# Optimization experiments

Measured on AMD Instinct MI355X. Metric: run time of the kernel, lower is better.

## Reference

```python
import jax, jax.numpy as jnp
import numpy as np
import math

B, S, E, H, L, FF = 32, 512, 256, 8, 4, 1024
DH = E // H
EPS = 1e-5


def layernorm(x):
    # nn.LayerNorm(elementwise_affine=False)
    m = jnp.mean(x, axis=-1, keepdims=True)
    v = jnp.mean((x - m) ** 2, axis=-1, keepdims=True)
    return (x - m) / jnp.sqrt(v + EPS)


def make_pos_embedding(e):
    vals = [math.sin(1 / 10000 ** ((i - 1) / e)) if i % 2 == 1
            else math.cos(i / 10000 ** ((i - 1) / e)) for i in range(e)]
    return jnp.asarray(np.array(vals, dtype=np.float32))


def setup_inputs() -> dict:
    key = jax.random.key(0)
    ks = jax.random.split(key, 8)
    sc = 0.02
    x = jax.random.normal(ks[0], (B, S, E), dtype=jnp.float32)
    Wq = jax.random.normal(ks[1], (L, H, DH, DH), dtype=jnp.float32) * sc
    Wk = jax.random.normal(ks[2], (L, H, DH, DH), dtype=jnp.float32) * sc
    Wv = jax.random.normal(ks[3], (L, H, DH, DH), dtype=jnp.float32) * sc
    W1 = jax.random.normal(ks[4], (L, E, FF), dtype=jnp.float32) * sc
    b1 = jnp.zeros((L, FF), dtype=jnp.float32)
    W2 = jax.random.normal(ks[5], (L, FF, E), dtype=jnp.float32) * sc
    b2 = jnp.zeros((L, E), dtype=jnp.float32)
    pos = make_pos_embedding(E)
    return {"x": x, "pos": pos, "Wq": Wq, "Wk": Wk, "Wv": Wv,
            "W1": W1, "b1": b1, "W2": W2, "b2": b2}


def encoder_layer(x, wq, wk, wv, w1, bb1, w2, bb2):
    xn = layernorm(x)
    xh = xn.reshape(B, S, H, DH)  # split embedding into per-head chunks
    q = jnp.einsum('bshd,hde->bhse', xh, wq)
    k = jnp.einsum('bshd,hde->bhse', xh, wk)
    v = jnp.einsum('bshd,hde->bhse', xh, wv)
    scores = jnp.einsum('bhsd,bhtd->bhst', q, k) / jnp.sqrt(jnp.float32(DH))
    a = jax.nn.softmax(scores, axis=-1)
    o = jnp.einsum('bhst,bhtd->bhsd', a, v)
    mha = o.transpose(0, 2, 1, 3).reshape(B, S, E)  # concat heads
    res = mha + x
    rn = layernorm(res)
    ffn = jax.nn.gelu(rn @ w1 + bb1, approximate=False) @ w2 + bb2
    return ffn + res


def reference(x, pos, Wq, Wk, Wv, W1, b1, W2, b2):
    h = x + pos  # fixed sinusoidal positional embedding
    for l in range(L):
        h = encoder_layer(h, Wq[l], Wk[l], Wv[l], W1[l], b1[l], W2[l], b2[l])
    return h
```

## Files before the change

### kernel.cpp

```cpp
#include <hip/hip_runtime.h>
#include <math.h>

#define BB   32
#define SS   512
#define EE   256
#define HH   8
#define LL   4
#define FFD  1024
#define DHD  32

constexpr float LN_EPS = 1e-5f;
constexpr int   NBSE   = BB * SS * EE;

typedef float  f32x4  __attribute__((ext_vector_type(4)));
typedef __bf16 bf16;
typedef __bf16 bf16x4 __attribute__((ext_vector_type(4)));
typedef __bf16 bf16x8 __attribute__((ext_vector_type(8)));

#define WAITV(n) asm volatile("s_waitcnt vmcnt(" #n ")" ::: "memory")

__device__ __forceinline__ void glds16(const bf16* g, bf16* l) {
    __builtin_amdgcn_global_load_lds(
        (const __attribute__((address_space(1))) void*)g,
        (__attribute__((address_space(3))) void*)l,
        16, 0, 0);
}

__device__ __forceinline__ float gelu_f(float x) {
    float u = x * x;
    float t = 1.5957691216057308f * x * (1.0f + 0.044715f * u);
    return x / (1.0f + __expf(-t));
}

__global__ __launch_bounds__(256) void k_prep(const float* __restrict__ W1,
                                              const float* __restrict__ W2,
                                              const float* __restrict__ Wq,
                                              const float* __restrict__ Wk,
                                              const float* __restrict__ Wv,
                                              bf16* __restrict__ W1t,
                                              bf16* __restrict__ W2t,
                                              bf16* __restrict__ Wqt,
                                              bf16* __restrict__ Wkt,
                                              bf16* __restrict__ Wvt) {
    __shared__ float tile[32][33];
    int bid = blockIdx.x;
    int tx = threadIdx.x & 31, ty = threadIdx.x >> 5;
    if (bid < 2048) {
        bool isw2 = bid >= 1024;
        int id = isw2 ? bid - 1024 : bid;
        int K = isw2 ? FFD : EE, N = isw2 ? EE : FFD;
        int l = id >> 8, rem = id & 255;
        int n0, k0;
        if (isw2) { n0 = (rem & 7) * 32;  k0 = (rem >> 3) * 32; }
        else      { n0 = (rem & 31) * 32; k0 = (rem >> 5) * 32; }
        const float* in = (isw2 ? W2 : W1) + (size_t)l * K * N;
        bf16* out       = (isw2 ? W2t : W1t) + (size_t)l * K * N;
        #pragma unroll
        for (int i = 0; i < 32; i += 8)
            tile[ty + i][tx] = in[(size_t)(k0 + ty + i) * N + n0 + tx];
        __syncthreads();
        #pragma unroll
        for (int i = 0; i < 32; i += 8)
            out[(size_t)(n0 + ty + i) * K + k0 + tx] = (bf16)tile[tx][ty + i];
    } else {
        int id = bid - 2048;
        int lh = id & 31, z = id >> 5;
        const float* in = (z == 0 ? Wq : z == 1 ? Wk : Wv) + (size_t)lh * 1024;
        bf16* out       = (z == 0 ? Wqt : z == 1 ? Wkt : Wvt) + (size_t)lh * 1024;
        float scale = (z == 0) ? 0.17677669529663687f : 1.0f;
        #pragma unroll
        for (int i = 0; i < 32; i += 8)
            tile[ty + i][tx] = in[(ty + i) * 32 + tx];
        __syncthreads();
        #pragma unroll
        for (int i = 0; i < 32; i += 8)
            out[(ty + i) * 32 + tx] = (bf16)(tile[tx][ty + i] * scale);
    }
}

template <bool ADDPOS>
__global__ __launch_bounds__(256) void k_lnqkv(const float* __restrict__ xin,
                                               const float* __restrict__ pos,
                                               float* __restrict__ hout,
                                               const bf16* __restrict__ Wqt,
                                               const bf16* __restrict__ Wkt,
                                               const bf16* __restrict__ Wvt,
                                               bf16* __restrict__ qb,
                                               bf16* __restrict__ kb,
                                               bf16* __restrict__ vb) {
    __shared__ __attribute__((aligned(16))) bf16 Xs[32 * 264];
    int b = blockIdx.x, s0 = blockIdx.y * 32;
    int tid = threadIdx.x, w = tid >> 6, lane = tid & 63;
    size_t rowoff = ((size_t)(b * SS + s0 + w * 8)) * EE + lane * 4;
    const float* hb = xin + rowoff;
    float4 pv;
    if (ADDPOS) pv = *(const float4*)(pos + lane * 4);
    float4 xr[8];
    #pragma unroll
    for (int i = 0; i < 8; i++)
        xr[i] = *(const float4*)(hb + (size_t)i * EE);
    if (ADDPOS) {
        #pragma unroll
        for (int i = 0; i < 8; i++) {
            xr[i].x += pv.x; xr[i].y += pv.y; xr[i].z += pv.z; xr[i].w += pv.w;
            *(float4*)(hout + rowoff + (size_t)i * EE) = xr[i];
        }
    }
    #pragma unroll
    for (int i = 0; i < 8; i++) {
        float4 v4 = xr[i];
        float sum = v4.x + v4.y + v4.z + v4.w;
        #pragma unroll
        for (int m = 1; m <= 32; m <<= 1) sum += __shfl_xor(sum, m, 64);
        float mean = sum * (1.0f / EE);
        float dx = v4.x - mean, dy = v4.y - mean, dz = v4.z - mean, dw = v4.w - mean;
        float ss = dx * dx + dy * dy + dz * dz + dw * dw;
        #pragma unroll
        for (int m = 1; m <= 32; m <<= 1) ss += __shfl_xor(ss, m, 64);
        float rstd = rsqrtf(ss * (1.0f / EE) + LN_EPS);
        bf16x4 o4 = { (bf16)(dx * rstd), (bf16)(dy * rstd), (bf16)(dz * rstd), (bf16)(dw * rstd) };
        *(bf16x4*)&Xs[(w * 8 + i) * 264 + lane * 4] = o4;
    }
    __syncthreads();
    int col = lane & 15, quad = lane >> 4;
    int rt = w & 1, hgrp = w >> 1;
    #pragma unroll
    for (int hh2 = 0; hh2 < 4; hh2++) {
        int h = hgrp * 4 + hh2;
        bf16x8 a = *(const bf16x8*)&Xs[(rt * 16 + col) * 264 + h * 32 + quad * 8];
        size_t base = ((size_t)((b * HH + h) * SS) + s0 + rt * 16) * DHD;
        #pragma unroll
        for (int nt = 0; nt < 2; nt++) {
            int e = nt * 16 + col;
            bf16x8 bq  = *(const bf16x8*)(Wqt + (h * 32 + e) * 32 + quad * 8);
            bf16x8 bk2 = *(const bf16x8*)(Wkt + (h * 32 + e) * 32 + quad * 8);
            bf16x8 bv2 = *(const bf16x8*)(Wvt + (h * 32 + e) * 32 + quad * 8);
            f32x4 z = {0.f, 0.f, 0.f, 0.f};
            f32x4 cq = __builtin_amdgcn_mfma_f32_16x16x32_bf16(bq, a, z, 0, 0, 0);
            f32x4 ck = __builtin_amdgcn_mfma_f32_16x16x32_bf16(bk2, a, z, 0, 0, 0);
            f32x4 cv = __builtin_amdgcn_mfma_f32_16x16x32_bf16(a, bv2, z, 0, 0, 0);
            bf16x4 q4 = { (bf16)cq[0], (bf16)cq[1], (bf16)cq[2], (bf16)cq[3] };
            bf16x4 k4 = { (bf16)ck[0], (bf16)ck[1], (bf16)ck[2], (bf16)ck[3] };
            size_t tb = base + (size_t)col * DHD + nt * 16 + quad * 4;
            *(bf16x4*)&qb[tb] = q4;
            *(bf16x4*)&kb[tb] = k4;
            bf16x4 vv = { (bf16)cv[0], (bf16)cv[1], (bf16)cv[2], (bf16)cv[3] };
            *(bf16x4*)&vb[(((size_t)(b * HH + h)) * DHD + e) * SS + s0 + rt * 16 + quad * 4] = vv;
        }
    }
}

#define ATT_LDK 40
#define ATT_LDV 264
#define ATT_LDP 36
__global__ __launch_bounds__(256) void k_attn(const bf16* __restrict__ Q,
                                              const bf16* __restrict__ K,
                                              const bf16* __restrict__ VT,
                                              bf16* __restrict__ O) {
    __shared__ __attribute__((aligned(16))) bf16 Ks[256 * ATT_LDK];
    __shared__ __attribute__((aligned(16))) bf16 Vs[32 * ATT_LDV];
    __shared__ __attribute__((aligned(16))) bf16 Ps[4][16 * ATT_LDP];
    int bh = blockIdx.x;
    int q0 = blockIdx.y * 128;
    int tid = threadIdx.x;
    int w = tid >> 6, lane = tid & 63;
    int col = lane & 15, quad = lane >> 4;
    bf16x8 aq[2];
    #pragma unroll
    for (int sub = 0; sub < 2; sub++)
        aq[sub] = *(const bf16x8*)(Q + ((size_t)(bh * SS + q0 + sub * 64 + w * 16 + col)) * DHD + quad * 8);
    float lr[2] = {0.f, 0.f};
    f32x4 oacc[2][2] = {};
    int ksr = tid >> 2, ksc = (tid & 3) * 8;
    int vd  = tid >> 5, vso = (tid & 31) * 8;
    bf16x8 kr[4], vr[4];
    #pragma unroll
    for (int it = 0; it < 4; it++) {
        kr[it] = *(const bf16x8*)(K + ((size_t)(bh * SS + it * 64 + ksr)) * DHD + ksc);
        vr[it] = *(const bf16x8*)(VT + (((size_t)bh * DHD + it * 8 + vd) * SS) + vso);
    }
    for (int ph = 0; ph < 2; ph++) {
        __syncthreads();
        #pragma unroll
        for (int it = 0; it < 4; it++) {
            *(bf16x8*)&Ks[(it * 64 + ksr) * ATT_LDK + ksc] = kr[it];
            *(bf16x8*)&Vs[(it * 8 + vd) * ATT_LDV + vso] = vr[it];
        }
        if (ph == 0) {
            #pragma unroll
            for (int it = 0; it < 4; it++) {
                kr[it] = *(const bf16x8*)(K + ((size_t)(bh * SS + 256 + it * 64 + ksr)) * DHD + ksc);
                vr[it] = *(const bf16x8*)(VT + (((size_t)bh * DHD + it * 8 + vd) * SS) + 256 + vso);
            }
        }
        __syncthreads();
        #pragma unroll
        for (int i = 0; i < 8; i++) {
            bf16x8 bk[2], bv[2];
            #pragma unroll
            for (int nt = 0; nt < 2; nt++) {
                bk[nt] = *(const bf16x8*)&Ks[(i * 32 + nt * 16 + col) * ATT_LDK + quad * 8];
                bv[nt] = *(const bf16x8*)&Vs[(nt * 16 + col) * ATT_LDV + i * 32 + quad * 8];
            }
            __builtin_amdgcn_s_setprio(1);
            #pragma unroll
            for (int sub = 0; sub < 2; sub++) {
                #pragma unroll
                for (int nt = 0; nt < 2; nt++) {
                    f32x4 z = {0.f, 0.f, 0.f, 0.f};
                    f32x4 st = __builtin_amdgcn_mfma_f32_16x16x32_bf16(bk[nt], aq[sub], z, 0, 0, 0);
                    bf16x4 p4;
                    #pragma unroll
                    for (int r = 0; r < 4; r++) {
                        float p = __expf(st[r]);
                        lr[sub] += p;
                        p4[r] = (bf16)p;
                    }
                    *(bf16x4*)&Ps[w][col * ATT_LDP + nt * 16 + quad * 4] = p4;
                }
                bf16x4 apl = *(const bf16x4*)&Ps[w][col * ATT_LDP + quad * 8];
                bf16x4 aph = *(const bf16x4*)&Ps[w][col * ATT_LDP + quad * 8 + 4];
                bf16x8 ap;
                ap[0] = apl[0]; ap[1] = apl[1]; ap[2] = apl[2]; ap[3] = apl[3];
                ap[4] = aph[0]; ap[5] = aph[1]; ap[6] = aph[2]; ap[7] = aph[3];
                #pragma unroll
                for (int nt = 0; nt < 2; nt++)
                    oacc[sub][nt] = __builtin_amdgcn_mfma_f32_16x16x32_bf16(ap, bv[nt], oacc[sub][nt], 0, 0, 0);
            }
            __builtin_amdgcn_s_setprio(0);
        }
    }
    int b = bh >> 3, hh = bh & 7;
    #pragma unroll
    for (int sub = 0; sub < 2; sub++) {
        float ls = lr[sub];
        ls += __shfl_xor(ls, 16, 64);
        ls += __shfl_xor(ls, 32, 64);
        #pragma unroll
        for (int r = 0; r < 4; r++) {
            float lrow = __shfl(ls, quad * 4 + r, 64);
            float inv = 1.0f / lrow;
            int row = q0 + sub * 64 + w * 16 + quad * 4 + r;
            size_t ob = ((size_t)(b * SS + row)) * EE + hh * 32;
            O[ob + col]      = (bf16)(oacc[sub][0][r] * inv);
            O[ob + 16 + col] = (bf16)(oacc[sub][1][r] * inv);
        }
    }
}

__global__ __launch_bounds__(256, 2) void k_ffn(const bf16* __restrict__ ob,
                                                const float* __restrict__ hb,
                                                const bf16* __restrict__ W1t_l,
                                                const float* __restrict__ b1_l,
                                                const bf16* __restrict__ W2t_l,
                                                const float* __restrict__ b2_l,
                                                float* __restrict__ Cf) {
    __shared__ __attribute__((aligned(16))) bf16 As[32 * 256];
    __shared__ __attribute__((aligned(16))) bf16 Gs[32 * 128];
    __shared__ __attribute__((aligned(16))) bf16 Bst[3][8192];
    __shared__ __attribute__((aligned(16))) float b1s[FFD];
    int tid = threadIdx.x, w = tid >> 6, lane = tid & 63;
    int col = lane & 15, quad = lane >> 4;
    int rg = w >> 1, cg = w & 1;
    int row0 = blockIdx.x * 32;

    int srow = tid >> 3;
    int spos = tid & 7;
    auto stage = [&](int g) {
        int ch = g >> 3, u = g & 7, slot = g % 3;
        if (u < 4) {
            #pragma unroll
            for (int i = 0; i < 4; i++) {
                int r = i * 32 + srow;
                glds16(W1t_l + (size_t)(ch * 128 + r) * EE + u * 64 + ((spos ^ (r & 7)) * 8),
                       &Bst[slot][i * 2048 + w * 512]);
            }
        } else {
            int j = (u - 4) >> 1, eh = (u - 4) & 1;
            #pragma unroll
            for (int i = 0; i < 4; i++) {
                int r = i * 32 + srow;
                glds16(W2t_l + (size_t)(eh * 128 + r) * FFD + ch * 128 + j * 64 + ((spos ^ (r & 7)) * 8),
                       &Bst[slot][i * 2048 + w * 512]);
            }
        }
    };
    stage(0);
    stage(1);
    stage(2);

    *(float4*)&b1s[tid * 4] = *(const float4*)&b1_l[tid * 4];

    #pragma unroll 2
    for (int rr = 0; rr < 8; rr++) {
        int r = w * 8 + rr;
        size_t g = (size_t)(row0 + r) * EE + lane * 4;
        float4 h4 = *(const float4*)(hb + g);
        bf16x4 o4 = *(const bf16x4*)(ob + g);
        float v0 = h4.x + (float)o4[0], v1 = h4.y + (float)o4[1];
        float v2 = h4.z + (float)o4[2], v3 = h4.w + (float)o4[3];
        float s1 = v0 + v1 + v2 + v3;
        float s2 = v0 * v0 + v1 * v1 + v2 * v2 + v3 * v3;
        #pragma unroll
        for (int m = 1; m <= 32; m <<= 1) {
            s1 += __shfl_xor(s1, m, 64);
            s2 += __shfl_xor(s2, m, 64);
        }
        float mean = s1 * (1.0f / EE);
        float rstd = rsqrtf(s2 * (1.0f / EE) - mean * mean + LN_EPS);
        bf16x4 a4 = { (bf16)((v0 - mean) * rstd), (bf16)((v1 - mean) * rstd),
                      (bf16)((v2 - mean) * rstd), (bf16)((v3 - mean) * rstd) };
        *(bf16x4*)&As[r * 256 + ((lane * 4) ^ ((r & 7) << 3))] = a4;
    }
    __syncthreads();

    f32x4 accO[8] = {};
    int ar = rg * 16 + col;
    int arx = (ar & 7) << 3;

    #pragma unroll
    for (int ch = 0; ch < 8; ch++) {
        f32x4 accG[4] = {};
        #pragma unroll
        for (int u = 0; u < 8; u++) {
            const int g = ch * 8 + u;
            const int slot = g % 3;
            if (g < 62) { WAITV(8); }
            else if (g == 62) { WAITV(4); }
            else { WAITV(0); }
            __builtin_amdgcn_s_barrier();
            if (u < 4) {
                bf16x8 af[2];
                #pragma unroll
                for (int kk = 0; kk < 2; kk++)
                    af[kk] = *(const bf16x8*)&As[ar * 256 + ((u * 64 + kk * 32 + quad * 8) ^ arx)];
                __builtin_amdgcn_s_setprio(1);
                #pragma unroll
                for (int nt = 0; nt < 4; nt++) {
                    int c = cg * 64 + nt * 16 + col;
                    #pragma unroll
                    for (int kk = 0; kk < 2; kk++) {
                        bf16x8 bfr = *(const bf16x8*)&Bst[slot][c * 64 + ((kk * 32 + quad * 8) ^ ((c & 7) << 3))];
                        accG[nt] = __builtin_amdgcn_mfma_f32_16x16x32_bf16(bfr, af[kk], accG[nt], 0, 0, 0);
                    }
                }
                __builtin_amdgcn_s_setprio(0);
                if (u == 3) {
                    #pragma unroll
                    for (int nt = 0; nt < 4; nt++) {
                        int f = cg * 64 + nt * 16 + quad * 4;
                        float4 b4 = *(const float4*)&b1s[ch * 128 + f];
                        bf16x4 g4;
                        g4[0] = (bf16)gelu_f(accG[nt][0] + b4.x);
                        g4[1] = (bf16)gelu_f(accG[nt][1] + b4.y);
                        g4[2] = (bf16)gelu_f(accG[nt][2] + b4.z);
                        g4[3] = (bf16)gelu_f(accG[nt][3] + b4.w);
                        *(bf16x4*)&Gs[ar * 128 + (f ^ arx)] = g4;
                    }
                    asm volatile("s_waitcnt lgkmcnt(0)" ::: "memory");
                }
            } else {
                const int j = (u - 4) >> 1, eh = (u - 4) & 1;
                bf16x8 af2[2];
                #pragma unroll
                for (int kk = 0; kk < 2; kk++)
                    af2[kk] = *(const bf16x8*)&Gs[ar * 128 + ((j * 64 + kk * 32 + quad * 8) ^ arx)];
                __builtin_amdgcn_s_setprio(1);
                #pragma unroll
                for (int nt = 0; nt < 4; nt++) {
                    int c = nt * 32 + cg * 16 + col;
                    #pragma unroll
                    for (int kk = 0; kk < 2; kk++) {
                        bf16x8 bfr = *(const bf16x8*)&Bst[slot][c * 64 + ((kk * 32 + quad * 8) ^ ((c & 7) << 3))];
                        accO[eh * 4 + nt] = __builtin_amdgcn_mfma_f32_16x16x32_bf16(bfr, af2[kk], accO[eh * 4 + nt], 0, 0, 0);
                    }
                }
                __builtin_amdgcn_s_setprio(0);
            }
            __builtin_amdgcn_s_barrier();
            if (g + 3 < 64) stage(g + 3);
        }
    }

    #pragma unroll
    for (int nta = 0; nta < 8; nta++) {
        int eh = nta >> 2;
        int row = row0 + rg * 16 + col;
        int cc = eh * 128 + (nta & 3) * 32 + cg * 16 + quad * 4;
        float4 b4 = *(const float4*)&b2_l[cc];
        float4 h4 = *(const float4*)&hb[(size_t)row * EE + cc];
        bf16x4 o4 = *(const bf16x4*)&ob[(size_t)row * EE + cc];
        float4 out;
        out.x = accO[nta][0] + b4.x + h4.x + (float)o4[0];
        out.y = accO[nta][1] + b4.y + h4.y + (float)o4[1];
        out.z = accO[nta][2] + b4.z + h4.z + (float)o4[2];
        out.w = accO[nta][3] + b4.w + h4.w + (float)o4[3];
        *(float4*)&Cf[(size_t)row * EE + cc] = out;
    }
}

extern "C" void kernel_launch(void* const* d_in, const int* in_sizes, int n_in,
                              void* d_out, int out_size, void* d_ws, size_t ws_size,
                              hipStream_t stream) {
    (void)in_sizes; (void)n_in; (void)out_size; (void)ws_size;
    const float* x   = (const float*)d_in[0];
    const float* pos = (const float*)d_in[1];
    const float* Wq  = (const float*)d_in[2];
    const float* Wk  = (const float*)d_in[3];
    const float* Wv  = (const float*)d_in[4];
    const float* W1  = (const float*)d_in[5];
    const float* b1  = (const float*)d_in[6];
    const float* W2  = (const float*)d_in[7];
    const float* b2  = (const float*)d_in[8];

    float* ws = (float*)d_ws;
    size_t N = (size_t)NBSE;
    float* h  = ws;
    bf16* ob  = (bf16*)(ws + N);
    bf16* qb  = (bf16*)(ws + 2 * N);
    bf16* kb  = qb + N;
    bf16* vb  = kb + N;
    bf16* W1t = (bf16*)(ws + 4 * N);
    bf16* W2t = W1t + (size_t)LL * EE * FFD;
    bf16* Wqt = W2t + (size_t)LL * EE * FFD;
    bf16* Wkt = Wqt + (size_t)LL * HH * DHD * DHD;
    bf16* Wvt = Wkt + (size_t)LL * HH * DHD * DHD;

    k_prep<<<2144, 256, 0, stream>>>(W1, W2, Wq, Wk, Wv, W1t, W2t, Wqt, Wkt, Wvt);
    for (int l = 0; l < LL; l++) {
        if (l == 0)
            k_lnqkv<true><<<dim3(BB, SS / 32), 256, 0, stream>>>(
                x, pos, h, Wqt, Wkt, Wvt, qb, kb, vb);
        else
            k_lnqkv<false><<<dim3(BB, SS / 32), 256, 0, stream>>>(
                h, nullptr, nullptr,
                Wqt + (size_t)l * HH * DHD * DHD, Wkt + (size_t)l * HH * DHD * DHD,
                Wvt + (size_t)l * HH * DHD * DHD, qb, kb, vb);
        k_attn<<<dim3(BB * HH, SS / 128), 256, 0, stream>>>(qb, kb, vb, ob);
        float* outp = (l == LL - 1) ? (float*)d_out : h;
        k_ffn<<<BB * SS / 32, 256, 0, stream>>>(
            ob, h, W1t + (size_t)l * FFD * EE, b1 + (size_t)l * FFD,
            W2t + (size_t)l * EE * FFD, b2 + (size_t)l * EE, outp);
    }
}
```

Baseline: 385.9 us.

## Software-pipeline LDS fragment reads ahead of MFMA in fused FFN loop

Restructures the fused FFN main loop so that each step's A and B operand fragments are read from LDS into registers during the previous step, right after the MFMAs. It also merges the two barriers per step into one, with the async global-to-LDS staging wait adjusted to match. The aim is to hide LDS read latency behind MFMA work and cut barrier overhead. In exchange it holds more fragment registers, which may cost occupancy, and relies on correct ordering of the waitcnt and barrier around the triple-buffered stages and the GELU writes to Gs.

```diff
diff --git a/kernel.cpp b/kernel.cpp
--- a/kernel.cpp
+++ b/kernel.cpp
@@ -312,74 +312,85 @@
                       (bf16)((v2 - mean) * rstd), (bf16)((v3 - mean) * rstd) };
         *(bf16x4*)&As[r * 256 + ((lane * 4) ^ ((r & 7) << 3))] = a4;
     }
+    WAITV(0);
     __syncthreads();
 
     f32x4 accO[8] = {};
+    f32x4 accG[4] = {};
     int ar = rg * 16 + col;
     int arx = (ar & 7) << 3;
 
-    #pragma unroll
-    for (int ch = 0; ch < 8; ch++) {
-        f32x4 accG[4] = {};
-        #pragma unroll
-        for (int u = 0; u < 8; u++) {
-            const int g = ch * 8 + u;
-            const int slot = g % 3;
-            if (g < 62) { WAITV(8); }
-            else if (g == 62) { WAITV(4); }
-            else { WAITV(0); }
-            __builtin_amdgcn_s_barrier();
-            if (u < 4) {
-                bf16x8 af[2];
+    bf16x8 fA[2], fB[8];
+    auto readA = [&](int gg) {
+        int u = gg & 7;
+        if (u < 4) {
+            #pragma unroll
+            for (int kk = 0; kk < 2; kk++)
+                fA[kk] = *(const bf16x8*)&As[ar * 256 + ((u * 64 + kk * 32 + quad * 8) ^ arx)];
+        } else {
+            int j = (u - 4) >> 1;
+            #pragma unroll
+            for (int kk = 0; kk < 2; kk++)
+                fA[kk] = *(const bf16x8*)&Gs[ar * 128 + ((j * 64 + kk * 32 + quad * 8) ^ arx)];
+        }
+    };
+    auto readB = [&](int gg) {
+        int u = gg & 7, slot = gg % 3;
+        #pragma unroll
+        for (int nt = 0; nt < 4; nt++) {
+            int c = (u < 4) ? (cg * 64 + nt * 16 + col) : (nt * 32 + cg * 16 + col);
+            #pragma unroll
+            for (int kk = 0; kk < 2; kk++)
+                fB[nt * 2 + kk] = *(const bf16x8*)&Bst[slot][c * 64 + ((kk * 32 + quad * 8) ^ ((c & 7) << 3))];
+        }
+    };
+    readB(0);
+    readA(0);
+
+    #pragma unroll
+    for (int g = 0; g < 64; g++) {
+        const int u = g & 7, ch = g >> 3;
+        __builtin_amdgcn_s_setprio(1);
+        if (u < 4) {
+            #pragma unroll
+            for (int nt = 0; nt < 4; nt++)
                 #pragma unroll
                 for (int kk = 0; kk < 2; kk++)
-                    af[kk] = *(const bf16x8*)&As[ar * 256 + ((u * 64 + kk * 32 + quad * 8) ^ arx)];
-                __builtin_amdgcn_s_setprio(1);
-                #pragma unroll
-                for (int nt = 0; nt < 4; nt++) {
-                    int c = cg * 64 + nt * 16 + col;
-                    #pragma unroll
-                    for (int kk = 0; kk < 2; kk++) {
-                        bf16x8 bfr = *(const bf16x8*)&Bst[slot][c * 64 + ((kk * 32 + quad * 8) ^ ((c & 7) << 3))];
-                        accG[nt] = __builtin_amdgcn_mfma_f32_16x16x32_bf16(bfr, af[kk], accG[nt], 0, 0, 0);
-                    }
-                }
-                __builtin_amdgcn_s_setprio(0);
-                if (u == 3) {
-                    #pragma unroll
-                    for (int nt = 0; nt < 4; nt++) {
-                        int f = cg * 64 + nt * 16 + quad * 4;
-                        float4 b4 = *(const float4*)&b1s[ch * 128 + f];
-                        bf16x4 g4;
-                        g4[0] = (bf16)gelu_f(accG[nt][0] + b4.x);
-                        g4[1] = (bf16)gelu_f(accG[nt][1] + b4.y);
-                        g4[2] = (bf16)gelu_f(accG[nt][2] + b4.z);
-                        g4[3] = (bf16)gelu_f(accG[nt][3] + b4.w);
-                        *(bf16x4*)&Gs[ar * 128 + (f ^ arx)] = g4;
-                    }
-                    asm volatile("s_waitcnt lgkmcnt(0)" ::: "memory");
-                }
-            } else {
-                const int j = (u - 4) >> 1, eh = (u - 4) & 1;
-                bf16x8 af2[2];
+                    accG[nt] = __builtin_amdgcn_mfma_f32_16x16x32_bf16(fB[nt * 2 + kk], fA[kk], accG[nt], 0, 0, 0);
+        } else {
+            const int eh = (u - 4) & 1;
+            #pragma unroll
+            for (int nt = 0; nt < 4; nt++)
                 #pragma unroll
                 for (int kk = 0; kk < 2; kk++)
-                    af2[kk] = *(const bf16x8*)&Gs[ar * 128 + ((j * 64 + kk * 32 + quad * 8) ^ arx)];
-                __builtin_amdgcn_s_setprio(1);
-                #pragma unroll
-                for (int nt = 0; nt < 4; nt++) {
-                    int c = nt * 32 + cg * 16 + col;
-                    #pragma unroll
-                    for (int kk = 0; kk < 2; kk++) {
-                        bf16x8 bfr = *(const bf16x8*)&Bst[slot][c * 64 + ((kk * 32 + quad * 8) ^ ((c & 7) << 3))];
-                        accO[eh * 4 + nt] = __builtin_amdgcn_mfma_f32_16x16x32_bf16(bfr, af2[kk], accO[eh * 4 + nt], 0, 0, 0);
-                    }
-                }
-                __builtin_amdgcn_s_setprio(0);
-            }
-            __builtin_amdgcn_s_barrier();
-            if (g + 3 < 64) stage(g + 3);
-        }
+                    accO[eh * 4 + nt] = __builtin_amdgcn_mfma_f32_16x16x32_bf16(fB[nt * 2 + kk], fA[kk], accO[eh * 4 + nt], 0, 0, 0);
+        }
+        __builtin_amdgcn_s_setprio(0);
+        if (u == 3) {
+            #pragma unroll
+            for (int nt = 0; nt < 4; nt++) {
+                int f = cg * 64 + nt * 16 + quad * 4;
+                float4 b4 = *(const float4*)&b1s[ch * 128 + f];
+                bf16x4 g4;
+                g4[0] = (bf16)gelu_f(accG[nt][0] + b4.x);
+                g4[1] = (bf16)gelu_f(accG[nt][1] + b4.y);
+                g4[2] = (bf16)gelu_f(accG[nt][2] + b4.z);
+                g4[3] = (bf16)gelu_f(accG[nt][3] + b4.w);
+                *(bf16x4*)&Gs[ar * 128 + (f ^ arx)] = g4;
+                f32x4 z = {0.f, 0.f, 0.f, 0.f};
+                accG[nt] = z;
+            }
+        }
+        if (g < 62)      { WAITV(4); }
+        else if (g == 62){ WAITV(0); }
+        if (g < 63) {
+            readB(g + 1);
+            if (((g + 1) & 7) != 4) readA(g + 1);
+        }
+        if (u == 3) asm volatile("s_waitcnt lgkmcnt(0)" ::: "memory");
+        __builtin_amdgcn_s_barrier();
+        if (g + 3 < 64) stage(g + 3);
+        if (g < 63 && ((g + 1) & 7) == 4) readA(g + 1);
     }
 
     #pragma unroll
```

Measured after the change: 494.0 us. 28.0% more time.
